# Optimization experiments

Hardware: AMD Instinct MI355X
Metric: run time of the kernel (lower is better)

The kernel has to match this reference:

```python
import jax, jax.numpy as jnp
import numpy as np

NEG_INF = -1e30  # stand-in for float('-inf') added to masked scores


def setup_inputs() -> dict:
    key = jax.random.key(0)
    ks = jax.random.split(key, 3)
    B, S, D = 4, 2048, 1024
    x = jax.random.normal(ks[0], (B, S, D), dtype=jnp.float32)
    W_qkv = jax.random.normal(ks[1], (D, 3 * D), dtype=jnp.float32) * (1.0 / np.sqrt(D))
    b_qkv = jnp.zeros((3 * D,), dtype=jnp.float32)
    W_out = jax.random.normal(ks[2], (D, D), dtype=jnp.float32) * (1.0 / np.sqrt(D))
    b_out = jnp.zeros((D,), dtype=jnp.float32)
    return {"x": x, "W_qkv": W_qkv, "b_qkv": b_qkv, "W_out": W_out, "b_out": b_out, "mask": 1}


def reference(x, W_qkv, b_qkv, W_out, b_out, mask):
    B, S, D = x.shape
    H = 16
    hd = D // H
    # fused QKV projection: [B,S,3D]
    qkv = x @ W_qkv + b_qkv
    # [B,S,H,3*hd] -> [B,H,S,3*hd], split into q,k,v each [B,H,S,hd]
    qkv = qkv.reshape(B, S, H, 3 * hd).transpose(0, 2, 1, 3)
    q, k, v = jnp.split(qkv, 3, axis=-1)
    # scaled dot-product attention, full score matrix [B,H,S,S]
    scaled = jnp.einsum('bhqd,bhkd->bhqk', q, k) / np.sqrt(hd)
    if mask:
        causal = jnp.triu(jnp.ones((S, S), dtype=bool), k=1)
        scaled = jnp.where(causal, NEG_INF, scaled)
    attention = jax.nn.softmax(scaled, axis=-1)
    values = jnp.einsum('bhqk,bhkd->bhqd', attention, v)
    # merge heads: [B,H,S,hd] -> [B,S,D] (matches tf.reshape on [B,H,S,hd])
    values = values.reshape(B, S, H * hd)
    return values @ W_out + b_out
```

## Files before the change

### kernel.cpp

```cpp
#include <hip/hip_runtime.h>
#include <hip/hip_bf16.h>

typedef __attribute__((ext_vector_type(8))) short short8;
typedef __attribute__((ext_vector_type(4))) float f32x4;

__device__ inline f32x4 mfma16(short8 a, short8 b, f32x4 c) {
    return __builtin_amdgcn_mfma_f32_16x16x32_bf16(a, b, c, 0, 0, 0);
}
__device__ inline short f2bf(float x) {
    __hip_bfloat16 h = __float2bfloat16(x);
    return *reinterpret_cast<short*>(&h);
}
__device__ inline unsigned short f2bfu(float x) {
    __hip_bfloat16 h = __float2bfloat16(x);
    return *reinterpret_cast<unsigned short*>(&h);
}
__device__ inline float bf2f(short u) {
    __hip_bfloat16 h = *reinterpret_cast<__hip_bfloat16*>(&u);
    return __bfloat162float(h);
}
__device__ inline float scrub(float v, float s) {
    return (fabsf(v) < 1e30f) ? v : s;
}
__device__ inline short8 scaleq(short8 v) {
    short8 r;
#pragma unroll
    for (int j = 0; j < 8; j++) r[j] = f2bf(bf2f(v[j]) * 0.125f);
    return r;
}

__global__ void detect_dtype(const unsigned short* __restrict__ x, int* flag) {
    __shared__ int cnt;
    if (threadIdx.x == 0) cnt = 0;
    __syncthreads();
    int c = 0;
    for (int i = threadIdx.x; i < 1024; i += 256) {
        unsigned short u = x[i];
        int e = (u >> 7) & 0xFF;
        if ((u & 0x7FFF) == 0 || (e >= 110 && e <= 143)) c++;
    }
    atomicAdd(&cnt, c);
    __syncthreads();
    if (threadIdx.x == 0) flag[0] = (cnt < 819) ? 1 : 0;
}

__global__ void conv_bias(const void* __restrict__ in, short* __restrict__ out,
                          int n, const int* __restrict__ flag) {
    int i = blockIdx.x * 256 + threadIdx.x;
    if (i >= n) return;
    out[i] = (*flag) ? f2bf(((const float*)in)[i]) : ((const short*)in)[i];
}

__global__ __launch_bounds__(256) void conv_x(const void* __restrict__ in,
                                              short* __restrict__ out, int n,
                                              const int* __restrict__ flag) {
    int i = (blockIdx.x * 256 + threadIdx.x) * 4;
    if (i >= n) return;
    if (*flag) {
        float4 f = *(const float4*)((const float*)in + i);
        unsigned int u0 = ((unsigned int)f2bfu(f.y) << 16) | f2bfu(f.x);
        unsigned int u1 = ((unsigned int)f2bfu(f.w) << 16) | f2bfu(f.z);
        *(uint2*)(out + i) = make_uint2(u0, u1);
    } else {
        *(uint2*)(out + i) = *(const uint2*)((const short*)in + i);
    }
}

__global__ void fill_sentinel(void* out, int n, const int* __restrict__ flag) {
    int i = blockIdx.x * 256 + threadIdx.x;
    if (i >= n) return;
    if (*flag) ((float*)out)[i] = 3e5f; else ((short*)out)[i] = f2bf(3e5f);
}

__global__ __launch_bounds__(256) void transpose_poly(const void* __restrict__ in,
                                                      short* __restrict__ out,
                                                      int R, int C,
                                                      const int* __restrict__ flag) {
    __shared__ short tile[32][33];
    const bool f32 = (*flag) != 0;
    int tx = threadIdx.x & 31, ty = threadIdx.x >> 5;
    int r0 = blockIdx.y * 32, c0 = blockIdx.x * 32;
#pragma unroll
    for (int i = 0; i < 4; i++) {
        size_t off = (size_t)(r0 + ty + i * 8) * C + c0 + tx;
        tile[ty + i * 8][tx] = f32 ? f2bf(((const float*)in)[off]) : ((const short*)in)[off];
    }
    __syncthreads();
#pragma unroll
    for (int i = 0; i < 4; i++)
        out[(size_t)(c0 + ty + i * 8) * R + r0 + tx] = tile[tx][ty + i * 8];
}

#define LDK 72

__global__ __launch_bounds__(256) void gemm_bt(const short* __restrict__ A,
                                               const short* __restrict__ Bt,
                                               const short* __restrict__ bias,
                                               void* __restrict__ Cv,
                                               int N, int K,
                                               const int* __restrict__ flag,
                                               int c_poly, float sent) {
    alignas(16) __shared__ short As[128 * LDK];
    alignas(16) __shared__ short Bs[128 * LDK];
    const bool cf32 = c_poly && (*flag);
    int tid = threadIdx.x;
    int wave = tid >> 6, lane = tid & 63;
    int lrow = lane & 15, lq = lane >> 4;
    int wm = (wave >> 1) * 64, wn = (wave & 1) * 64;
    int m0 = blockIdx.y * 128, n0 = blockIdx.x * 128;

    f32x4 acc[4][4];
#pragma unroll
    for (int i = 0; i < 4; i++)
#pragma unroll
        for (int j = 0; j < 4; j++) acc[i][j] = (f32x4){0.f, 0.f, 0.f, 0.f};

    int srow = tid >> 3;
    int scol = (tid & 7) * 8;

    for (int kb = 0; kb < K; kb += 64) {
#pragma unroll
        for (int p = 0; p < 4; p++) {
            int row = p * 32 + srow;
            *(short8*)&As[row * LDK + scol] =
                *(const short8*)&A[(size_t)(m0 + row) * K + kb + scol];
            *(short8*)&Bs[row * LDK + scol] =
                *(const short8*)&Bt[(size_t)(n0 + row) * K + kb + scol];
        }
        __syncthreads();
#pragma unroll
        for (int ks = 0; ks < 2; ks++) {
            short8 af[4], bf[4];
#pragma unroll
            for (int i = 0; i < 4; i++)
                af[i] = *(short8*)&As[(wm + i * 16 + lrow) * LDK + ks * 32 + lq * 8];
#pragma unroll
            for (int i = 0; i < 4; i++)
                bf[i] = *(short8*)&Bs[(wn + i * 16 + lrow) * LDK + ks * 32 + lq * 8];
#pragma unroll
            for (int i = 0; i < 4; i++)
#pragma unroll
                for (int j = 0; j < 4; j++)
                    acc[i][j] = mfma16(af[i], bf[j], acc[i][j]);
        }
        __syncthreads();
    }

    const __hip_bfloat16* bias16 = (const __hip_bfloat16*)bias;
#pragma unroll
    for (int j = 0; j < 4; j++) {
        int col = n0 + wn + j * 16 + lrow;
        float bv = __bfloat162float(bias16[col]);
#pragma unroll
        for (int i = 0; i < 4; i++) {
            int rbase = m0 + wm + i * 16 + lq * 4;
#pragma unroll
            for (int r = 0; r < 4; r++) {
                float val = scrub(acc[i][j][r] + bv, sent);
                size_t off = (size_t)(rbase + r) * N + col;
                if (cf32) ((float*)Cv)[off] = val; else ((short*)Cv)[off] = f2bf(val);
            }
        }
    }
}

#define VP2 72
#define PP 72

__global__ __launch_bounds__(256) void attn_kernel(const short* __restrict__ QKV,
                                                   short* __restrict__ AO,
                                                   const int* __restrict__ maskp) {
    constexpr int S = 2048, C3 = 3072;
    alignas(16) __shared__ short Vt[2][64 * VP2];
    alignas(16) __shared__ short Pt[4][2][16 * PP];

    int tid = threadIdx.x;
    int wave = tid >> 6, lane = tid & 63;
    int lrow = lane & 15, lq = lane >> 4;
    int bh = blockIdx.y;
    const bool causal = (*maskp) != 0;
    const short* base = QKV + (size_t)(bh >> 4) * S * C3 + (bh & 15) * 192;

    int vi2 = (tid & 31) * 2;
    int vd0 = (tid >> 5) * 8;

    int buf = 0;
    for (int tile = 0; tile < 2; tile++) {
        int q0t = (tile == 0) ? blockIdx.x * 128 : 1920 - blockIdx.x * 128;

        int qg[2];
        short8 qf0[2], qf1[2];
#pragma unroll
        for (int g = 0; g < 2; g++) {
            qg[g] = q0t + wave * 32 + g * 16 + lrow;
            qf0[g] = scaleq(*(const short8*)(base + (size_t)qg[g] * C3 + lq * 8));
            qf1[g] = scaleq(*(const short8*)(base + (size_t)qg[g] * C3 + 32 + lq * 8));
        }

        float m_i[2] = {-1e38f, -1e38f}, l_i[2] = {0.f, 0.f};
        f32x4 acc[2][4];
#pragma unroll
        for (int g = 0; g < 2; g++)
#pragma unroll
            for (int nt = 0; nt < 4; nt++) acc[g][nt] = (f32x4){0.f, 0.f, 0.f, 0.f};

        int nkv = causal ? (q0t + 128) : S;

        for (int kv0 = 0; kv0 < nkv; kv0 += 64) {
            {
                const short* vs0 = base + (size_t)(kv0 + vi2) * C3 + 128 + vd0;
                union { short8 v; unsigned short u[8]; } a, b;
                a.v = *(const short8*)vs0;
                b.v = *(const short8*)(vs0 + C3);
                unsigned int* vt = (unsigned int*)&Vt[buf][0];
#pragma unroll
                for (int j = 0; j < 8; j++)
                    vt[((vd0 + j) * VP2 + vi2) >> 1] =
                        ((unsigned int)b.u[j] << 16) | a.u[j];
            }
            __syncthreads();

            f32x4 s[2][4];
#pragma unroll
            for (int sub = 0; sub < 4; sub++) {
                const short* kb = base + (size_t)(kv0 + sub * 16 + lrow) * C3 + 64;
                short8 kf0 = *(const short8*)(kb + lq * 8);
                short8 kf1 = *(const short8*)(kb + 32 + lq * 8);
#pragma unroll
                for (int g = 0; g < 2; g++) {
                    f32x4 a = (f32x4){0.f, 0.f, 0.f, 0.f};
                    a = mfma16(kf0, qf0[g], a);
                    a = mfma16(kf1, qf1[g], a);
                    s[g][sub] = a;
                }
            }

#pragma unroll
            for (int g = 0; g < 2; g++) {
                if (causal && (kv0 + 63 > q0t + wave * 32 + g * 16)) {
#pragma unroll
                    for (int sub = 0; sub < 4; sub++) {
                        int kvg = kv0 + sub * 16 + lq * 4;
#pragma unroll
                        for (int r = 0; r < 4; r++)
                            if (kvg + r > qg[g]) s[g][sub][r] = -1e30f;
                    }
                }
                float vmax = -1e38f;
#pragma unroll
                for (int sub = 0; sub < 4; sub++) {
                    float a = fmaxf(fmaxf(s[g][sub][0], s[g][sub][1]),
                                    fmaxf(s[g][sub][2], s[g][sub][3]));
                    vmax = fmaxf(vmax, a);
                }
                vmax = fmaxf(vmax, __shfl_xor(vmax, 16, 64));
                vmax = fmaxf(vmax, __shfl_xor(vmax, 32, 64));
                float mnew = fmaxf(m_i[g], vmax);
                float alpha = __expf(m_i[g] - mnew);
                float lsum = 0.f;
                unsigned int pk[4][2];
#pragma unroll
                for (int sub = 0; sub < 4; sub++) {
                    float p0 = __expf(s[g][sub][0] - mnew);
                    float p1 = __expf(s[g][sub][1] - mnew);
                    float p2 = __expf(s[g][sub][2] - mnew);
                    float p3 = __expf(s[g][sub][3] - mnew);
                    lsum += (p0 + p1) + (p2 + p3);
                    pk[sub][0] = ((unsigned int)f2bfu(p1) << 16) | f2bfu(p0);
                    pk[sub][1] = ((unsigned int)f2bfu(p3) << 16) | f2bfu(p2);
                }
                lsum += __shfl_xor(lsum, 16, 64);
                lsum += __shfl_xor(lsum, 32, 64);
                l_i[g] = l_i[g] * alpha + lsum;
                m_i[g] = mnew;
#pragma unroll
                for (int nt = 0; nt < 4; nt++)
#pragma unroll
                    for (int r = 0; r < 4; r++) acc[g][nt][r] *= alpha;
                unsigned int* pt = (unsigned int*)&Pt[wave][g][0];
#pragma unroll
                for (int sub = 0; sub < 4; sub++)
                    *(uint2*)&pt[(lrow * PP + sub * 16 + lq * 4) >> 1] =
                        make_uint2(pk[sub][0], pk[sub][1]);
            }

#pragma unroll
            for (int ks = 0; ks < 2; ks++) {
                short8 pfA = *(short8*)&Pt[wave][0][lrow * PP + ks * 32 + lq * 8];
                short8 pfB = *(short8*)&Pt[wave][1][lrow * PP + ks * 32 + lq * 8];
#pragma unroll
                for (int nt = 0; nt < 4; nt++) {
                    short8 vf = *(short8*)&Vt[buf][(nt * 16 + lrow) * VP2 + ks * 32 + lq * 8];
                    acc[0][nt] = mfma16(vf, pfA, acc[0][nt]);
                    acc[1][nt] = mfma16(vf, pfB, acc[1][nt]);
                }
            }
            buf ^= 1;
        }

#pragma unroll
        for (int g = 0; g < 2; g++) {
            float inv = 1.f / l_i[g];
            short* ob = AO + ((size_t)bh * S + qg[g]) * 64;
#pragma unroll
            for (int nt = 0; nt < 4; nt++) {
                unsigned int u0 = ((unsigned int)f2bfu(scrub(acc[g][nt][1] * inv, 4e4f)) << 16) |
                                  f2bfu(scrub(acc[g][nt][0] * inv, 4e4f));
                unsigned int u1 = ((unsigned int)f2bfu(scrub(acc[g][nt][3] * inv, 4e4f)) << 16) |
                                  f2bfu(scrub(acc[g][nt][2] * inv, 4e4f));
                *(uint2*)(ob + nt * 16 + lq * 4) = make_uint2(u0, u1);
            }
        }
    }
}

extern "C" void kernel_launch(void* const* d_in, const int* in_sizes, int n_in,
                              void* d_out, int out_size, void* d_ws, size_t ws_size,
                              hipStream_t stream) {
    char* ws = (char*)d_ws;
    int*   flag  = (int*)ws;
    short* bq_bf = (short*)(ws + 65536);
    short* bo_bf = (short*)(ws + 131072);
    short* WqkvT = (short*)(ws + (1ull << 20));
    short* WoutT = (short*)(ws + 7ull * (1ull << 20));
    short* xbfAO = (short*)(ws + 9ull * (1ull << 20));
    short* QKVc  = (short*)(ws + 25ull * (1ull << 20));

    detect_dtype<<<1, 256, 0, stream>>>((const unsigned short*)d_in[0], flag);

    if (ws_size < 73ull * 1048576) {
        fill_sentinel<<<(8388608 + 255) / 256, 256, 0, stream>>>(d_out, 8388608, flag);
        return;
    }

    conv_bias<<<12, 256, 0, stream>>>(d_in[2], bq_bf, 3072, flag);
    conv_bias<<<4, 256, 0, stream>>>(d_in[4], bo_bf, 1024, flag);
    transpose_poly<<<dim3(96, 32), 256, 0, stream>>>(d_in[1], WqkvT, 1024, 3072, flag);
    transpose_poly<<<dim3(32, 32), 256, 0, stream>>>(d_in[3], WoutT, 1024, 1024, flag);
    conv_x<<<8192, 256, 0, stream>>>(d_in[0], xbfAO, 8388608, flag);

    gemm_bt<<<dim3(24, 64), 256, 0, stream>>>(xbfAO, WqkvT, bq_bf, QKVc,
                                              3072, 1024, flag, 0, 8e4f);
    attn_kernel<<<dim3(8, 64), 256, 0, stream>>>(QKVc, xbfAO, (const int*)d_in[5]);
    gemm_bt<<<dim3(8, 64), 256, 0, stream>>>(xbfAO, WoutT, bo_bf, d_out,
                                             1024, 1024, flag, 1, 2e4f);
}
```

Measured before the change: 328.3 us.

## Prefetch next K/V tile into registers and skip rescale when max stable

Software-pipelines the attention loop by loading the next 64-row K and V fragments from global memory into registers while the current tile is computed, hiding global load latency. It also adds a lazy online-softmax rescale that skips the alpha multiply of the accumulator and running sum when the wave's new max does not exceed the old one by more than 8. Launch bounds now request two blocks per CU. The extra prefetch registers raise register pressure under the tighter occupancy bound, and the lazy rescale lets exp values grow up to e^8 before bf16 packing.

```diff
diff --git a/kernel.cpp b/kernel.cpp
--- a/kernel.cpp
+++ b/kernel.cpp
@@ -167,9 +167,9 @@
 #define VP2 72
 #define PP 72
 
-__global__ __launch_bounds__(256) void attn_kernel(const short* __restrict__ QKV,
-                                                   short* __restrict__ AO,
-                                                   const int* __restrict__ maskp) {
+__global__ __launch_bounds__(256, 2) void attn_kernel(const short* __restrict__ QKV,
+                                                      short* __restrict__ AO,
+                                                      const int* __restrict__ maskp) {
     constexpr int S = 2048, C3 = 3072;
     alignas(16) __shared__ short Vt[2][64 * VP2];
     alignas(16) __shared__ short Pt[4][2][16 * PP];
@@ -206,12 +206,23 @@
 
         int nkv = causal ? (q0t + 128) : S;
 
+        short8 va, vb, kf0[4], kf1[4];
+        {
+            const short* vs0 = base + (size_t)vi2 * C3 + 128 + vd0;
+            va = *(const short8*)vs0;
+            vb = *(const short8*)(vs0 + C3);
+#pragma unroll
+            for (int sub = 0; sub < 4; sub++) {
+                const short* kb = base + (size_t)(sub * 16 + lrow) * C3 + 64;
+                kf0[sub] = *(const short8*)(kb + lq * 8);
+                kf1[sub] = *(const short8*)(kb + 32 + lq * 8);
+            }
+        }
+
         for (int kv0 = 0; kv0 < nkv; kv0 += 64) {
             {
-                const short* vs0 = base + (size_t)(kv0 + vi2) * C3 + 128 + vd0;
                 union { short8 v; unsigned short u[8]; } a, b;
-                a.v = *(const short8*)vs0;
-                b.v = *(const short8*)(vs0 + C3);
+                a.v = va; b.v = vb;
                 unsigned int* vt = (unsigned int*)&Vt[buf][0];
 #pragma unroll
                 for (int j = 0; j < 8; j++)
@@ -220,17 +231,28 @@
             }
             __syncthreads();
 
+            int kvn = (kv0 + 64 < nkv) ? kv0 + 64 : kv0;
+            short8 va_n, vb_n, kf0_n[4], kf1_n[4];
+            {
+                const short* vs0 = base + (size_t)(kvn + vi2) * C3 + 128 + vd0;
+                va_n = *(const short8*)vs0;
+                vb_n = *(const short8*)(vs0 + C3);
+#pragma unroll
+                for (int sub = 0; sub < 4; sub++) {
+                    const short* kb = base + (size_t)(kvn + sub * 16 + lrow) * C3 + 64;
+                    kf0_n[sub] = *(const short8*)(kb + lq * 8);
+                    kf1_n[sub] = *(const short8*)(kb + 32 + lq * 8);
+                }
+            }
+
             f32x4 s[2][4];
 #pragma unroll
             for (int sub = 0; sub < 4; sub++) {
-                const short* kb = base + (size_t)(kv0 + sub * 16 + lrow) * C3 + 64;
-                short8 kf0 = *(const short8*)(kb + lq * 8);
-                short8 kf1 = *(const short8*)(kb + 32 + lq * 8);
 #pragma unroll
                 for (int g = 0; g < 2; g++) {
                     f32x4 a = (f32x4){0.f, 0.f, 0.f, 0.f};
-                    a = mfma16(kf0, qf0[g], a);
-                    a = mfma16(kf1, qf1[g], a);
+                    a = mfma16(kf0[sub], qf0[g], a);
+                    a = mfma16(kf1[sub], qf1[g], a);
                     s[g][sub] = a;
                 }
             }
@@ -242,8 +264,8 @@
                     for (int sub = 0; sub < 4; sub++) {
                         int kvg = kv0 + sub * 16 + lq * 4;
 #pragma unroll
-                        for (int r = 0; r < 4; r++)
-                            if (kvg + r > qg[g]) s[g][sub][r] = -1e30f;
+                        for (int rr = 0; rr < 4; rr++)
+                            if (kvg + rr > qg[g]) s[g][sub][rr] = -1e30f;
                     }
                 }
                 float vmax = -1e38f;
@@ -255,8 +277,16 @@
                 }
                 vmax = fmaxf(vmax, __shfl_xor(vmax, 16, 64));
                 vmax = fmaxf(vmax, __shfl_xor(vmax, 32, 64));
-                float mnew = fmaxf(m_i[g], vmax);
-                float alpha = __expf(m_i[g] - mnew);
+                float mnew = m_i[g];
+                if (!__all(vmax <= m_i[g] + 8.0f)) {
+                    mnew = fmaxf(m_i[g], vmax);
+                    float alpha = __expf(m_i[g] - mnew);
+                    l_i[g] *= alpha;
+#pragma unroll
+                    for (int nt = 0; nt < 4; nt++)
+#pragma unroll
+                        for (int rr = 0; rr < 4; rr++) acc[g][nt][rr] *= alpha;
+                }
                 float lsum = 0.f;
                 unsigned int pk[4][2];
 #pragma unroll
@@ -271,12 +301,8 @@
                 }
                 lsum += __shfl_xor(lsum, 16, 64);
                 lsum += __shfl_xor(lsum, 32, 64);
-                l_i[g] = l_i[g] * alpha + lsum;
+                l_i[g] += lsum;
                 m_i[g] = mnew;
-#pragma unroll
-                for (int nt = 0; nt < 4; nt++)
-#pragma unroll
-                    for (int r = 0; r < 4; r++) acc[g][nt][r] *= alpha;
                 unsigned int* pt = (unsigned int*)&Pt[wave][g][0];
 #pragma unroll
                 for (int sub = 0; sub < 4; sub++)
@@ -294,6 +320,13 @@
                     acc[0][nt] = mfma16(vf, pfA, acc[0][nt]);
                     acc[1][nt] = mfma16(vf, pfB, acc[1][nt]);
                 }
+            }
+
+            va = va_n; vb = vb_n;
+#pragma unroll
+            for (int sub = 0; sub < 4; sub++) {
+                kf0[sub] = kf0_n[sub];
+                kf1[sub] = kf1_n[sub];
             }
             buf ^= 1;
         }
```

Measured after the change: 314.5 us. -4.2%, faster.
